# Kernel tuning notes

Measured on AMD Instinct MI355X. Metric: run time of the kernel, lower is better.

## Reference

```python
import jax, jax.numpy as jnp
import numpy as np

N_NODES = 50000
N_EDGES = 600000
IN_CH = 300
HID = 128
N_CLASSES = 2
N_GRAPHS = 128
BN_EPS = 1e-5


def setup_inputs() -> dict:
    key = jax.random.key(0)
    ks = jax.random.split(key, 24)
    x = jax.random.normal(ks[0], (N_NODES, IN_CH), dtype=jnp.float32)
    edge_index = jax.random.randint(ks[1], (2, N_EDGES), 0, N_NODES, dtype=jnp.int64)
    batch = jnp.sort(jax.random.randint(ks[2], (N_NODES,), 0, N_GRAPHS, dtype=jnp.int64))

    def glorot(k, shape):
        fan_in, fan_out = shape
        s = jnp.sqrt(2.0 / (fan_in + fan_out)).astype(jnp.float32)
        return jax.random.normal(k, shape, dtype=jnp.float32) * s

    inp = {"x": x, "edge_index": edge_index, "batch": batch}
    # SAGEConv params: W_l (neighbor branch), W_r (root branch), bias
    dims = [(IN_CH, HID), (HID, HID), (HID, HID)]
    for i, (din, dout) in enumerate(dims, start=1):
        inp[f"W{i}l"] = glorot(ks[3 * i], (din, dout))
        inp[f"W{i}r"] = glorot(ks[3 * i + 1], (din, dout))
        inp[f"b{i}"] = jnp.zeros((dout,), dtype=jnp.float32)
        inp[f"g{i}"] = jnp.ones((dout,), dtype=jnp.float32)   # BN gamma
        inp[f"be{i}"] = jnp.zeros((dout,), dtype=jnp.float32)  # BN beta
    inp["Wc"] = glorot(ks[20], (HID, N_CLASSES))
    inp["bc"] = jnp.zeros((N_CLASSES,), dtype=jnp.float32)
    return inp


def _sage_conv(x, src, dst, Wl, Wr, b):
    # mean-aggregate neighbor features (messages flow src -> dst)
    msg_sum = jax.ops.segment_sum(x[src], dst, num_segments=N_NODES)
    deg = jax.ops.segment_sum(jnp.ones((src.shape[0],), dtype=x.dtype), dst,
                              num_segments=N_NODES)
    mean = msg_sum / jnp.maximum(deg, 1.0)[:, None]
    return mean @ Wl + x @ Wr + b


def _bn_relu(h, gamma, beta):
    mu = jnp.mean(h, axis=0)
    var = jnp.var(h, axis=0)
    h = (h - mu) * jax.lax.rsqrt(var + BN_EPS) * gamma + beta
    return jax.nn.relu(h)


def reference(x, edge_index, batch,
              W1l, W1r, b1, g1, be1,
              W2l, W2r, b2, g2, be2,
              W3l, W3r, b3, g3, be3,
              Wc, bc):
    src, dst = edge_index[0], edge_index[1]
    h = _bn_relu(_sage_conv(x, src, dst, W1l, W1r, b1), g1, be1)
    h = _bn_relu(_sage_conv(h, src, dst, W2l, W2r, b2), g2, be2)
    h = _bn_relu(_sage_conv(h, src, dst, W3l, W3r, b3), g3, be3)
    # global mean pool per graph
    pooled = jax.ops.segment_sum(h, batch, num_segments=N_GRAPHS)
    cnt = jax.ops.segment_sum(jnp.ones((h.shape[0],), dtype=h.dtype), batch,
                              num_segments=N_GRAPHS)
    hg = pooled / jnp.maximum(cnt, 1.0)[:, None]
    out = hg @ Wc + bc
    return out, hg
```

## Files before the change

kernel.cpp:

```cpp
#include <hip/hip_runtime.h>

#define N_NODES   50000
#define N_EDGES   600000
#define IN_CH     300
#define HID       128
#define N_CLASSES 2
#define N_GRAPHS  128
#define BN_EPS    1e-5f

#define NB ((N_NODES + 511) / 512)
#define KP1 320
#define NREP 32
#define DEGB ((N_EDGES + 255) / 256)

typedef __attribute__((ext_vector_type(8))) short bf8_t;
typedef __attribute__((ext_vector_type(4))) float f4_t;

__device__ __forceinline__ unsigned short f2bf(float x) {
    union { float f; unsigned u; } q; q.f = x;
    unsigned r = q.u + 0x7fffu + ((q.u >> 16) & 1u);
    return (unsigned short)(r >> 16);
}
__device__ __forceinline__ float bf2f(unsigned short h) {
    union { float f; unsigned u; } q; q.u = ((unsigned)h) << 16; return q.f;
}

__device__ __forceinline__ void async_cp16(const void* g, void* l) {
    __builtin_amdgcn_global_load_lds(
        (const __attribute__((address_space(1))) unsigned int*)g,
        (__attribute__((address_space(3))) unsigned int*)l, 16, 0, 0);
}

__global__ __launch_bounds__(256) void deg_prepw(const int* __restrict__ dst,
                                                 int* __restrict__ ideg,
                                                 const float* __restrict__ W1l,
                                                 const float* __restrict__ W1r,
                                                 const float* __restrict__ W2l,
                                                 const float* __restrict__ W2r,
                                                 const float* __restrict__ W3l,
                                                 const float* __restrict__ W3r,
                                                 unsigned short* __restrict__ B1h,
                                                 unsigned short* __restrict__ B1l,
                                                 unsigned short* __restrict__ B2h,
                                                 unsigned short* __restrict__ B2l,
                                                 unsigned short* __restrict__ B3h,
                                                 unsigned short* __restrict__ B3l) {
    int b = blockIdx.x;
    if (b < DEGB) {
        int e = b * 256 + threadIdx.x;
        if (e < N_EDGES) atomicAdd(&ideg[dst[e]], 1);
        return;
    }
    int pb = b - DEGB;
    int layer, base;
    if (pb < 320)      { layer = 0; base = pb; }
    else if (pb < 448) { layer = 1; base = pb - 320; }
    else               { layer = 2; base = pb - 448; }
    int Kp = (layer == 0) ? KP1 : HID;
    int K  = (layer == 0) ? IN_CH : HID;
    const float* Wl = (layer == 0) ? W1l : ((layer == 1) ? W2l : W3l);
    const float* Wr = (layer == 0) ? W1r : ((layer == 1) ? W2r : W3r);
    unsigned short* Bh = (layer == 0) ? B1h : ((layer == 1) ? B2h : B3h);
    unsigned short* Bl = (layer == 0) ? B1l : ((layer == 1) ? B2l : B3l);
    int idx = base * 256 + threadIdx.x;
    int n = idx / Kp;
    int k = idx - n * Kp;
    float v = 0.f;
    if (k < K) v = (n < 128) ? Wl[k * 128 + n] : Wr[k * 128 + (n - 128)];
    unsigned short h = f2bf(v);
    unsigned short l = f2bf(v - bf2f(h));
    Bh[idx] = h;
    Bl[idx] = l;
}

__global__ __launch_bounds__(256) void scan_fused(const int* __restrict__ ideg,
                                                  int* __restrict__ row_start,
                                                  float* __restrict__ invdeg,
                                                  int* __restrict__ bsum,
                                                  int* __restrict__ bflag) {
    int b = blockIdx.x, t = threadIdx.x;
    int lane = t & 63, wv = t >> 6;
    int i0 = b * 512 + t * 2;
    int v0 = 0, v1 = 0;
    if (i0 < N_NODES) {
        int2 v = *(const int2*)&ideg[i0];
        v0 = v.x; v1 = v.y;
    }
    int tot = v0 + v1;
    int s = tot;
#pragma unroll
    for (int d = 1; d < 64; d <<= 1) {
        int u = __shfl_up(s, d);
        if (lane >= d) s += u;
    }
    __shared__ int ws[4];
    if (lane == 63) ws[wv] = s;
    __syncthreads();
    int btot = ws[0] + ws[1] + ws[2] + ws[3];
    if (t == 0) {
        atomicExch(&bsum[b], btot);
        __threadfence();
        atomicExch(&bflag[b], 1);
    }
    int part = 0;
    if (t < b) {
        while (atomicAdd(&bflag[t], 0) == 0) {}
        part = atomicAdd(&bsum[t], 0);
    }
#pragma unroll
    for (int d = 1; d < 64; d <<= 1) part += __shfl_down(part, d);
    __shared__ int ps[4];
    if (lane == 0) ps[wv] = part;
    __syncthreads();
    int boff = ps[0] + ps[1] + ps[2] + ps[3];
    int woff = 0;
    for (int w = 0; w < wv; ++w) woff += ws[w];
    int base = boff + woff + (s - tot);
    if (i0 < N_NODES) {
        row_start[i0]     = base;
        row_start[i0 + 1] = base + v0;
        invdeg[i0]     = 1.0f / fmaxf((float)v0, 1.0f);
        invdeg[i0 + 1] = 1.0f / fmaxf((float)v1, 1.0f);
    }
    if (t == 0 && b == NB - 1) row_start[N_NODES] = boff + btot;
}

__global__ __launch_bounds__(256) void fill_kernel(const int* __restrict__ src,
                                                   const int* __restrict__ dst,
                                                   const int* __restrict__ row_start,
                                                   int* __restrict__ cursor,
                                                   int* __restrict__ csr_src) {
    int e = blockIdx.x * 256 + threadIdx.x;
    if (e >= N_EDGES) return;
    int d = dst[e];
    int pos = row_start[d] + atomicAdd(&cursor[d], 1);
    csr_src[pos] = src[e];
}

__global__ __launch_bounds__(256) void gemm_mfma_x(const float* __restrict__ X,
                                                   int M,
                                                   const unsigned short* __restrict__ Bhi,
                                                   const unsigned short* __restrict__ Blo,
                                                   const float* __restrict__ bias,
                                                   unsigned short* __restrict__ C0,
                                                   float* __restrict__ C1) {
    __shared__ __align__(16) unsigned short sAh[2][64 * 32];
    __shared__ __align__(16) unsigned short sAl[2][64 * 32];
    __shared__ __align__(16) unsigned short sBh[2][256 * 32];
    __shared__ __align__(16) unsigned short sBl[2][256 * 32];

    const int tid  = threadIdx.x;
    const int lane = tid & 63;
    const int wave = tid >> 6;
    const int l16  = lane & 15;
    const int quad = lane >> 4;
    const long m0  = (long)blockIdx.x * 64;
    const int  n0  = wave * 64;

    f4_t acc[4][4];
#pragma unroll
    for (int mt = 0; mt < 4; ++mt)
#pragma unroll
        for (int nt = 0; nt < 4; ++nt) acc[mt][nt] = (f4_t){0.f, 0.f, 0.f, 0.f};

    const int ar  = tid >> 2;
    const int cl  = tid & 3;
    const int cpa = cl ^ ((ar >> 1) & 3);
    long agr = m0 + ar;
    if (agr >= M) agr = M - 1;
    const float* gX = X + agr * IN_CH;

    const int cg = ((lane & 3) ^ ((lane >> 3) & 3)) * 8;
    const unsigned short* gBh[4];
    const unsigned short* gBl[4];
    int lBo[4];
#pragma unroll
    for (int j = 0; j < 4; ++j) {
        long br = wave * 64 + j * 16 + (lane >> 2);
        gBh[j] = Bhi + br * KP1 + cg;
        gBl[j] = Blo + br * KP1 + cg;
        lBo[j] = wave * 2048 + j * 512;
    }
    const int rsw = (quad ^ ((l16 >> 1) & 3)) * 8;

    auto copyB = [&](int k0, int buf) {
#pragma unroll
        for (int j = 0; j < 4; ++j) {
            async_cp16(gBh[j] + k0, &sBh[buf][lBo[j]]);
            async_cp16(gBl[j] + k0, &sBl[buf][lBo[j]]);
        }
    };
    auto loadA = [&](int k0, float4& a0, float4& a1) {
        int gk = k0 + cl * 8;
        a0 = (gk + 4 <= IN_CH) ? *(const float4*)(gX + gk)
                               : make_float4(0.f, 0.f, 0.f, 0.f);
        a1 = (gk + 8 <= IN_CH) ? *(const float4*)(gX + gk + 4)
                               : make_float4(0.f, 0.f, 0.f, 0.f);
    };
    auto storeA = [&](int buf, float4 a0, float4 a1) {
        float f[8];
        f[0] = a0.x; f[1] = a0.y; f[2] = a0.z; f[3] = a0.w;
        f[4] = a1.x; f[5] = a1.y; f[6] = a1.z; f[7] = a1.w;
        bf8_t h8, l8;
#pragma unroll
        for (int j = 0; j < 8; ++j) {
            unsigned short h = f2bf(f[j]);
            h8[j] = (short)h;
            l8[j] = (short)f2bf(f[j] - bf2f(h));
        }
        *(bf8_t*)&sAh[buf][ar * 32 + cpa * 8] = h8;
        *(bf8_t*)&sAl[buf][ar * 32 + cpa * 8] = l8;
    };

    {
        float4 a0, a1;
        loadA(0, a0, a1);
        copyB(0, 0);
        storeA(0, a0, a1);
    }
    __syncthreads();

    const int NT = KP1 / 32;
    int cur = 0;
    for (int t = 0; t < NT; ++t) {
        float4 na0 = make_float4(0.f, 0.f, 0.f, 0.f);
        float4 na1 = make_float4(0.f, 0.f, 0.f, 0.f);
        const bool more = (t + 1 < NT);
        if (more) {
            loadA((t + 1) * 32, na0, na1);
            copyB((t + 1) * 32, cur ^ 1);
        }

        bf8_t ah[4], al[4];
#pragma unroll
        for (int mt = 0; mt < 4; ++mt) {
            ah[mt] = *(const bf8_t*)&sAh[cur][(mt * 16 + l16) * 32 + rsw];
            al[mt] = *(const bf8_t*)&sAl[cur][(mt * 16 + l16) * 32 + rsw];
        }
#pragma unroll
        for (int nt = 0; nt < 4; ++nt) {
            bf8_t bh = *(const bf8_t*)&sBh[cur][(n0 + nt * 16 + l16) * 32 + rsw];
            bf8_t bl = *(const bf8_t*)&sBl[cur][(n0 + nt * 16 + l16) * 32 + rsw];
#pragma unroll
            for (int mt = 0; mt < 4; ++mt) {
                acc[mt][nt] = __builtin_amdgcn_mfma_f32_16x16x32_bf16(ah[mt], bh, acc[mt][nt], 0, 0, 0);
                acc[mt][nt] = __builtin_amdgcn_mfma_f32_16x16x32_bf16(al[mt], bh, acc[mt][nt], 0, 0, 0);
                acc[mt][nt] = __builtin_amdgcn_mfma_f32_16x16x32_bf16(ah[mt], bl, acc[mt][nt], 0, 0, 0);
            }
        }

        if (more) storeA(cur ^ 1, na0, na1);
        __syncthreads();
        cur ^= 1;
    }

    const bool left = (n0 < 128);
    if (left) {
        int ncol[4];
#pragma unroll
        for (int nt = 0; nt < 4; ++nt) ncol[nt] = n0 + nt * 16 + l16;
#pragma unroll
        for (int mt = 0; mt < 4; ++mt)
#pragma unroll
            for (int r = 0; r < 4; ++r) {
                long row = m0 + mt * 16 + quad * 4 + r;
                if (row < M) {
#pragma unroll
                    for (int nt = 0; nt < 4; ++nt)
                        C0[row * 128 + ncol[nt]] = f2bf(acc[mt][nt][r]);
                }
            }
    } else {
        float badd[4];
        int   ncol[4];
#pragma unroll
        for (int nt = 0; nt < 4; ++nt) {
            int ng = n0 + nt * 16 + l16 - 128;
            ncol[nt] = ng;
            badd[nt] = bias[ng];
        }
#pragma unroll
        for (int mt = 0; mt < 4; ++mt)
#pragma unroll
            for (int r = 0; r < 4; ++r) {
                long row = m0 + mt * 16 + quad * 4 + r;
                if (row < M) {
#pragma unroll
                    for (int nt = 0; nt < 4; ++nt)
                        C1[row * 128 + ncol[nt]] = acc[mt][nt][r] + badd[nt];
                }
            }
    }
}

__global__ __launch_bounds__(256) void gemm_mfma_h(const float* __restrict__ Hpre,
                                                   int M,
                                                   const float* __restrict__ rep,
                                                   const float* __restrict__ gamma,
                                                   const float* __restrict__ beta,
                                                   const unsigned short* __restrict__ Bhi,
                                                   const unsigned short* __restrict__ Blo,
                                                   const float* __restrict__ bias,
                                                   unsigned short* __restrict__ C0,
                                                   float* __restrict__ C1) {
    __shared__ __align__(16) unsigned short sAh[64 * 32];
    __shared__ __align__(16) unsigned short sAl[64 * 32];
    __shared__ __align__(16) unsigned short sBh[2][256 * 32];
    __shared__ __align__(16) unsigned short sBl[2][256 * 32];
    __shared__ float sSC[256];

    const int tid  = threadIdx.x;
    const int lane = tid & 63;
    const int wave = tid >> 6;
    const int l16  = lane & 15;
    const int quad = lane >> 4;
    const long m0  = (long)blockIdx.x * 64;
    const int  n0  = wave * 64;

    {
        float* S = (float*)sAh;
        float a = 0.f;
#pragma unroll
        for (int r = 0; r < NREP; ++r) a += rep[r * 256 + tid];
        S[tid] = a;
        __syncthreads();
        if (tid < HID) {
            const float invn = 1.0f / (float)N_NODES;
            float mu  = S[tid] * invn;
            float var = S[HID + tid] * invn - mu * mu;
            float sc  = gamma[tid] * rsqrtf(var + BN_EPS);
            sSC[tid]       = sc;
            sSC[HID + tid] = beta[tid] - mu * sc;
        }
        __syncthreads();
    }

    f4_t acc[4][4];
#pragma unroll
    for (int mt = 0; mt < 4; ++mt)
#pragma unroll
        for (int nt = 0; nt < 4; ++nt) acc[mt][nt] = (f4_t){0.f, 0.f, 0.f, 0.f};

    const int ar  = tid >> 2;
    const int cl  = tid & 3;
    const int cpa = cl ^ ((ar >> 1) & 3);
    long agr = m0 + ar;
    if (agr >= M) agr = M - 1;
    const float* gH = Hpre + agr * HID;

    const int cg = ((lane & 3) ^ ((lane >> 3) & 3)) * 8;
    const unsigned short* gBh[4];
    const unsigned short* gBl[4];
    int lBo[4];
#pragma unroll
    for (int j = 0; j < 4; ++j) {
        long br = wave * 64 + j * 16 + (lane >> 2);
        gBh[j] = Bhi + br * HID + cg;
        gBl[j] = Blo + br * HID + cg;
        lBo[j] = wave * 2048 + j * 512;
    }
    const int rsw = (quad ^ ((l16 >> 1) & 3)) * 8;

    auto copyB = [&](int k0, int buf) {
#pragma unroll
        for (int j = 0; j < 4; ++j) {
            async_cp16(gBh[j] + k0, &sBh[buf][lBo[j]]);
            async_cp16(gBl[j] + k0, &sBl[buf][lBo[j]]);
        }
    };
    auto loadA = [&](int k0, float4& a0, float4& a1) {
        int gk = k0 + cl * 8;
        a0 = *(const float4*)(gH + gk);
        a1 = *(const float4*)(gH + gk + 4);
    };
    auto storeA = [&](int k0, float4 v0, float4 v1) {
        const int gk = k0 + cl * 8;
        float4 s0 = *(const float4*)&sSC[gk];
        float4 s1 = *(const float4*)&sSC[gk + 4];
        float4 t0 = *(const float4*)&sSC[HID + gk];
        float4 t1 = *(const float4*)&sSC[HID + gk + 4];
        float f[8];
        f[0] = fmaxf(v0.x * s0.x + t0.x, 0.f);
        f[1] = fmaxf(v0.y * s0.y + t0.y, 0.f);
        f[2] = fmaxf(v0.z * s0.z + t0.z, 0.f);
        f[3] = fmaxf(v0.w * s0.w + t0.w, 0.f);
        f[4] = fmaxf(v1.x * s1.x + t1.x, 0.f);
        f[5] = fmaxf(v1.y * s1.y + t1.y, 0.f);
        f[6] = fmaxf(v1.z * s1.z + t1.z, 0.f);
        f[7] = fmaxf(v1.w * s1.w + t1.w, 0.f);
        bf8_t h8, l8;
#pragma unroll
        for (int j = 0; j < 8; ++j) {
            unsigned short h = f2bf(f[j]);
            h8[j] = (short)h;
            l8[j] = (short)f2bf(f[j] - bf2f(h));
        }
        *(bf8_t*)&sAh[ar * 32 + cpa * 8] = h8;
        *(bf8_t*)&sAl[ar * 32 + cpa * 8] = l8;
    };

    {
        float4 a0, a1;
        loadA(0, a0, a1);
        copyB(0, 0);
        storeA(0, a0, a1);
    }
    __syncthreads();

    int cur = 0;
#pragma unroll
    for (int t = 0; t < 4; ++t) {
        float4 na0 = make_float4(0.f, 0.f, 0.f, 0.f);
        float4 na1 = make_float4(0.f, 0.f, 0.f, 0.f);
        const bool more = (t < 3);
        if (more) {
            loadA((t + 1) * 32, na0, na1);
            copyB((t + 1) * 32, cur ^ 1);
        }

        bf8_t ah[4], al[4];
#pragma unroll
        for (int mt = 0; mt < 4; ++mt) {
            ah[mt] = *(const bf8_t*)&sAh[(mt * 16 + l16) * 32 + rsw];
            al[mt] = *(const bf8_t*)&sAl[(mt * 16 + l16) * 32 + rsw];
        }
#pragma unroll
        for (int nt = 0; nt < 4; ++nt) {
            bf8_t bh = *(const bf8_t*)&sBh[cur][(n0 + nt * 16 + l16) * 32 + rsw];
            bf8_t bl = *(const bf8_t*)&sBl[cur][(n0 + nt * 16 + l16) * 32 + rsw];
#pragma unroll
            for (int mt = 0; mt < 4; ++mt) {
                acc[mt][nt] = __builtin_amdgcn_mfma_f32_16x16x32_bf16(ah[mt], bh, acc[mt][nt], 0, 0, 0);
                acc[mt][nt] = __builtin_amdgcn_mfma_f32_16x16x32_bf16(al[mt], bh, acc[mt][nt], 0, 0, 0);
                acc[mt][nt] = __builtin_amdgcn_mfma_f32_16x16x32_bf16(ah[mt], bl, acc[mt][nt], 0, 0, 0);
            }
        }

        __syncthreads();
        if (more) storeA((t + 1) * 32, na0, na1);
        __syncthreads();
        cur ^= 1;
    }

    const bool left = (n0 < 128);
    if (left) {
        int ncol[4];
#pragma unroll
        for (int nt = 0; nt < 4; ++nt) ncol[nt] = n0 + nt * 16 + l16;
#pragma unroll
        for (int mt = 0; mt < 4; ++mt)
#pragma unroll
            for (int r = 0; r < 4; ++r) {
                long row = m0 + mt * 16 + quad * 4 + r;
                if (row < M) {
#pragma unroll
                    for (int nt = 0; nt < 4; ++nt)
                        C0[row * 128 + ncol[nt]] = f2bf(acc[mt][nt][r]);
                }
            }
    } else {
        float badd[4];
        int   ncol[4];
#pragma unroll
        for (int nt = 0; nt < 4; ++nt) {
            int ng = n0 + nt * 16 + l16 - 128;
            ncol[nt] = ng;
            badd[nt] = bias[ng];
        }
#pragma unroll
        for (int mt = 0; mt < 4; ++mt)
#pragma unroll
            for (int r = 0; r < 4; ++r) {
                long row = m0 + mt * 16 + quad * 4 + r;
                if (row < M) {
#pragma unroll
                    for (int nt = 0; nt < 4; ++nt)
                        C1[row * 128 + ncol[nt]] = acc[mt][nt][r] + badd[nt];
                }
            }
    }
}

__global__ __launch_bounds__(256) void gather_agg(const unsigned short* __restrict__ Pl,
                                                  const int* __restrict__ row_start,
                                                  const int* __restrict__ csr_src,
                                                  const float* __restrict__ invdeg,
                                                  float* __restrict__ out,
                                                  float* __restrict__ rep) {
    int slot = threadIdx.x >> 5;
    int lane = threadIdx.x & 31;
    int node = blockIdx.x * 8 + slot;
    int beg = row_start[node];
    int end = row_start[node + 1];
    const unsigned short* base = Pl + lane * 4;
    float sx = 0.f, sy = 0.f, sz = 0.f, sw = 0.f;
    int j = beg;
    for (; j + 8 <= end; j += 8) {
        int idx[8];
#pragma unroll
        for (int u = 0; u < 8; ++u) idx[u] = csr_src[j + u];
        ushort4 v[8];
#pragma unroll
        for (int u = 0; u < 8; ++u) v[u] = *(const ushort4*)(base + (long)idx[u] * HID);
#pragma unroll
        for (int u = 0; u < 8; ++u) {
            sx += bf2f(v[u].x); sy += bf2f(v[u].y);
            sz += bf2f(v[u].z); sw += bf2f(v[u].w);
        }
    }
    if (j + 4 <= end) {
        int idx[4];
#pragma unroll
        for (int u = 0; u < 4; ++u) idx[u] = csr_src[j + u];
        ushort4 v[4];
#pragma unroll
        for (int u = 0; u < 4; ++u) v[u] = *(const ushort4*)(base + (long)idx[u] * HID);
#pragma unroll
        for (int u = 0; u < 4; ++u) {
            sx += bf2f(v[u].x); sy += bf2f(v[u].y);
            sz += bf2f(v[u].z); sw += bf2f(v[u].w);
        }
        j += 4;
    }
    for (; j < end; ++j) {
        int i0 = csr_src[j];
        ushort4 v0 = *(const ushort4*)(base + (long)i0 * HID);
        sx += bf2f(v0.x); sy += bf2f(v0.y); sz += bf2f(v0.z); sw += bf2f(v0.w);
    }
    float w = invdeg[node];
    float* o = out + (long)node * HID + lane * 4;
    float4 cur = *(float4*)o;
    cur.x += sx * w;
    cur.y += sy * w;
    cur.z += sz * w;
    cur.w += sw * w;
    *(float4*)o = cur;

    __shared__ float red[8][HID];
    float* repb = rep + (blockIdx.x & (NREP - 1)) * 256;
    *(float4*)&red[slot][lane * 4] = make_float4(cur.x, cur.y, cur.z, cur.w);
    __syncthreads();
    if (threadIdx.x < HID) {
        float tsum = 0.f;
#pragma unroll
        for (int s = 0; s < 8; ++s) tsum += red[s][threadIdx.x];
        atomicAdd(&repb[threadIdx.x], tsum);
    }
    __syncthreads();
    *(float4*)&red[slot][lane * 4] = make_float4(cur.x * cur.x, cur.y * cur.y,
                                                 cur.z * cur.z, cur.w * cur.w);
    __syncthreads();
    if (threadIdx.x < HID) {
        float tsum = 0.f;
#pragma unroll
        for (int s = 0; s < 8; ++s) tsum += red[s][threadIdx.x];
        atomicAdd(&repb[HID + threadIdx.x], tsum);
    }
}

__global__ __launch_bounds__(1024) void poolhead_bn(const float* __restrict__ h,
                                                    const int* __restrict__ batch,
                                                    const float* __restrict__ rep,
                                                    const float* __restrict__ gamma,
                                                    const float* __restrict__ beta,
                                                    const float* __restrict__ Wc,
                                                    const float* __restrict__ bc,
                                                    float* __restrict__ out) {
    __shared__ float S[256];
    __shared__ float SC[256];
    int g = blockIdx.x;
    int t = threadIdx.x;
    int c = t & 127;
    int half = t >> 7;
    if (t < 256) {
        float a = 0.f;
#pragma unroll
        for (int r = 0; r < NREP; ++r) a += rep[r * 256 + t];
        S[t] = a;
    }
    __shared__ int lo_sh, hi_sh;
    if (t == 0) {
        int lo = 0, hi = N_NODES;
        while (lo < hi) { int m = (lo + hi) >> 1; if (batch[m] < g) lo = m + 1; else hi = m; }
        lo_sh = lo;
        int lo2 = lo, hi2 = N_NODES;
        while (lo2 < hi2) { int m = (lo2 + hi2) >> 1; if (batch[m] < g + 1) lo2 = m + 1; else hi2 = m; }
        hi_sh = lo2;
    }
    __syncthreads();
    if (t < HID) {
        const float invn = 1.0f / (float)N_NODES;
        float mu  = S[t] * invn;
        float var = S[HID + t] * invn - mu * mu;
        float sc  = gamma[t] * rsqrtf(var + BN_EPS);
        SC[t]       = sc;
        SC[HID + t] = beta[t] - mu * sc;
    }
    __syncthreads();
    float bsc = SC[c], bsh = SC[HID + c];
    int lo = lo_sh, hi = hi_sh;
    float a0 = 0.f, a1 = 0.f, a2 = 0.f, a3 = 0.f;
    int r = lo + half;
    for (; r + 24 < hi; r += 32) {
        a0 += fmaxf(h[(long)(r +  0) * HID + c] * bsc + bsh, 0.f);
        a1 += fmaxf(h[(long)(r +  8) * HID + c] * bsc + bsh, 0.f);
        a2 += fmaxf(h[(long)(r + 16) * HID + c] * bsc + bsh, 0.f);
        a3 += fmaxf(h[(long)(r + 24) * HID + c] * bsc + bsh, 0.f);
    }
    for (; r < hi; r += 8) a0 += fmaxf(h[(long)r * HID + c] * bsc + bsh, 0.f);
    __shared__ float red[8][HID];
    red[half][c] = (a0 + a1) + (a2 + a3);
    __syncthreads();
    __shared__ float r0[HID], r1[HID];
    if (t < HID) {
        float inv = 1.0f / fmaxf((float)(hi - lo), 1.0f);
        float v = 0.f;
#pragma unroll
        for (int s = 0; s < 8; ++s) v += red[s][t];
        v *= inv;
        out[N_GRAPHS * N_CLASSES + g * HID + t] = v;
        r0[t] = v * Wc[t * 2 + 0];
        r1[t] = v * Wc[t * 2 + 1];
    }
    __syncthreads();
    if (t < 2) {
        const float* rr = t ? r1 : r0;
        float sum = bc[t];
        for (int i = 0; i < HID; ++i) sum += rr[i];
        out[g * 2 + t] = sum;
    }
}

extern "C" void kernel_launch(void* const* d_in, const int* in_sizes, int n_in,
                              void* d_out, int out_size, void* d_ws, size_t ws_size,
                              hipStream_t stream) {
    const float* x     = (const float*)d_in[0];
    const int*   ei    = (const int*)d_in[1];
    const int*   batch = (const int*)d_in[2];
    const float* W1l = (const float*)d_in[3];
    const float* W1r = (const float*)d_in[4];
    const float* b1  = (const float*)d_in[5];
    const float* g1  = (const float*)d_in[6];
    const float* be1 = (const float*)d_in[7];
    const float* W2l = (const float*)d_in[8];
    const float* W2r = (const float*)d_in[9];
    const float* b2  = (const float*)d_in[10];
    const float* g2  = (const float*)d_in[11];
    const float* be2 = (const float*)d_in[12];
    const float* W3l = (const float*)d_in[13];
    const float* W3r = (const float*)d_in[14];
    const float* b3  = (const float*)d_in[15];
    const float* g3  = (const float*)d_in[16];
    const float* be3 = (const float*)d_in[17];
    const float* Wc  = (const float*)d_in[18];
    const float* bc  = (const float*)d_in[19];

    const int* src = ei;
    const int* dst = ei + N_EDGES;

    float* ws = (float*)d_ws;
    const long FEAT = (long)N_NODES * HID;
    unsigned short* Pl16 = (unsigned short*)ws;
    float* buf1 = ws + FEAT;
    float* buf2 = ws + 2 * FEAT;
    int*   ideg      = (int*)(ws + 3 * FEAT);
    int*   cursor    = ideg + N_NODES;
    int*   bsum      = cursor + N_NODES;
    int*   bflag     = bsum + 128;
    int*   row_start = bflag + 128;
    int*   csr_src   = row_start + N_NODES + 4;
    float* invdeg    = (float*)(csr_src + N_EDGES);
    float* reps      = invdeg + N_NODES;
    unsigned short* B1h = (unsigned short*)(reps + 3 * NREP * 256);
    unsigned short* B1l = B1h + 256 * KP1;
    unsigned short* B2h = B1l + 256 * KP1;
    unsigned short* B2l = B2h + 256 * HID;
    unsigned short* B3h = B2l + 256 * HID;
    unsigned short* B3l = B3h + 256 * HID;

    float* outp = (float*)d_out;

    const int gemm_grid   = (N_NODES + 63) / 64;
    const int gather_grid = N_NODES / 8;
    const int dp_grid     = DEGB + 320 + 128 + 128;

    hipMemsetAsync(ideg, 0, (2 * N_NODES + 256) * sizeof(int), stream);
    hipMemsetAsync(reps, 0, 3 * NREP * 256 * sizeof(float), stream);

    deg_prepw<<<dp_grid, 256, 0, stream>>>(dst, ideg, W1l, W1r, W2l, W2r, W3l, W3r,
                                           B1h, B1l, B2h, B2l, B3h, B3l);
    scan_fused<<<NB, 256, 0, stream>>>(ideg, row_start, invdeg, bsum, bflag);
    fill_kernel<<<(N_EDGES + 255) / 256, 256, 0, stream>>>(src, dst, row_start, cursor, csr_src);

    gemm_mfma_x<<<gemm_grid, 256, 0, stream>>>(x, N_NODES, B1h, B1l, b1, Pl16, buf1);
    gather_agg<<<gather_grid, 256, 0, stream>>>(Pl16, row_start, csr_src, invdeg, buf1, reps);

    gemm_mfma_h<<<gemm_grid, 256, 0, stream>>>(buf1, N_NODES, reps, g1, be1,
                                               B2h, B2l, b2, Pl16, buf2);
    gather_agg<<<gather_grid, 256, 0, stream>>>(Pl16, row_start, csr_src, invdeg, buf2, reps + NREP * 256);

    gemm_mfma_h<<<gemm_grid, 256, 0, stream>>>(buf2, N_NODES, reps + NREP * 256, g2, be2,
                                               B3h, B3l, b3, Pl16, buf1);
    gather_agg<<<gather_grid, 256, 0, stream>>>(Pl16, row_start, csr_src, invdeg, buf1, reps + 2 * NREP * 256);

    poolhead_bn<<<N_GRAPHS, 1024, 0, stream>>>(buf1, batch, reps + 2 * NREP * 256,
                                               g3, be3, Wc, bc, outp);
}
```

Baseline: 404.1 us.

## Pre-swizzle weights into MFMA fragment layout and load B directly from global

```diff
diff --git a/kernel.cpp b/kernel.cpp
--- a/kernel.cpp
+++ b/kernel.cpp
@@ -23,12 +23,6 @@
 }
 __device__ __forceinline__ float bf2f(unsigned short h) {
     union { float f; unsigned u; } q; q.u = ((unsigned)h) << 16; return q.f;
-}
-
-__device__ __forceinline__ void async_cp16(const void* g, void* l) {
-    __builtin_amdgcn_global_load_lds(
-        (const __attribute__((address_space(1))) unsigned int*)g,
-        (__attribute__((address_space(3))) unsigned int*)l, 16, 0, 0);
 }
 
 __global__ __launch_bounds__(256) void deg_prepw(const int* __restrict__ dst,
@@ -69,8 +63,15 @@
     if (k < K) v = (n < 128) ? Wl[k * 128 + n] : Wr[k * 128 + (n - 128)];
     unsigned short h = f2bf(v);
     unsigned short l = f2bf(v - bf2f(h));
-    Bh[idx] = h;
-    Bl[idx] = l;
+    int NST   = Kp >> 5;
+    int ntile = n >> 4;
+    int l16n  = n & 15;
+    int kstep = k >> 5;
+    int kk    = k & 31;
+    int lane2 = (kk >> 3) * 16 + l16n;
+    int addr  = ((ntile * NST + kstep) * 64 + lane2) * 8 + (kk & 7);
+    Bh[addr] = h;
+    Bl[addr] = l;
 }
 
 __global__ __launch_bounds__(256) void scan_fused(const int* __restrict__ ideg,
@@ -146,8 +147,6 @@
                                                    float* __restrict__ C1) {
     __shared__ __align__(16) unsigned short sAh[2][64 * 32];
     __shared__ __align__(16) unsigned short sAl[2][64 * 32];
-    __shared__ __align__(16) unsigned short sBh[2][256 * 32];
-    __shared__ __align__(16) unsigned short sBl[2][256 * 32];
 
     const int tid  = threadIdx.x;
     const int lane = tid & 63;
@@ -170,26 +169,12 @@
     if (agr >= M) agr = M - 1;
     const float* gX = X + agr * IN_CH;
 
-    const int cg = ((lane & 3) ^ ((lane >> 3) & 3)) * 8;
-    const unsigned short* gBh[4];
-    const unsigned short* gBl[4];
-    int lBo[4];
-#pragma unroll
-    for (int j = 0; j < 4; ++j) {
-        long br = wave * 64 + j * 16 + (lane >> 2);
-        gBh[j] = Bhi + br * KP1 + cg;
-        gBl[j] = Blo + br * KP1 + cg;
-        lBo[j] = wave * 2048 + j * 512;
-    }
     const int rsw = (quad ^ ((l16 >> 1) & 3)) * 8;
-
-    auto copyB = [&](int k0, int buf) {
-#pragma unroll
-        for (int j = 0; j < 4; ++j) {
-            async_cp16(gBh[j] + k0, &sBh[buf][lBo[j]]);
-            async_cp16(gBl[j] + k0, &sBl[buf][lBo[j]]);
-        }
-    };
+    const int NT  = KP1 / 32;
+
+    const bf8_t* Bh0 = (const bf8_t*)Bhi;
+    const bf8_t* Bl0 = (const bf8_t*)Blo;
+
     auto loadA = [&](int k0, float4& a0, float4& a1) {
         int gk = k0 + cl * 8;
         a0 = (gk + 4 <= IN_CH) ? *(const float4*)(gX + gk)
@@ -215,20 +200,23 @@
     {
         float4 a0, a1;
         loadA(0, a0, a1);
-        copyB(0, 0);
         storeA(0, a0, a1);
     }
     __syncthreads();
 
-    const int NT = KP1 / 32;
     int cur = 0;
     for (int t = 0; t < NT; ++t) {
         float4 na0 = make_float4(0.f, 0.f, 0.f, 0.f);
         float4 na1 = make_float4(0.f, 0.f, 0.f, 0.f);
         const bool more = (t + 1 < NT);
-        if (more) {
-            loadA((t + 1) * 32, na0, na1);
-            copyB((t + 1) * 32, cur ^ 1);
+        if (more) loadA((t + 1) * 32, na0, na1);
+
+        bf8_t bhv[4], blv[4];
+#pragma unroll
+        for (int nt = 0; nt < 4; ++nt) {
+            long bi = ((long)(wave * 4 + nt) * NT + t) * 64 + lane;
+            bhv[nt] = Bh0[bi];
+            blv[nt] = Bl0[bi];
         }
 
         bf8_t ah[4], al[4];
@@ -239,13 +227,11 @@
         }
 #pragma unroll
         for (int nt = 0; nt < 4; ++nt) {
-            bf8_t bh = *(const bf8_t*)&sBh[cur][(n0 + nt * 16 + l16) * 32 + rsw];
-            bf8_t bl = *(const bf8_t*)&sBl[cur][(n0 + nt * 16 + l16) * 32 + rsw];
 #pragma unroll
             for (int mt = 0; mt < 4; ++mt) {
-                acc[mt][nt] = __builtin_amdgcn_mfma_f32_16x16x32_bf16(ah[mt], bh, acc[mt][nt], 0, 0, 0);
-                acc[mt][nt] = __builtin_amdgcn_mfma_f32_16x16x32_bf16(al[mt], bh, acc[mt][nt], 0, 0, 0);
-                acc[mt][nt] = __builtin_amdgcn_mfma_f32_16x16x32_bf16(ah[mt], bl, acc[mt][nt], 0, 0, 0);
+                acc[mt][nt] = __builtin_amdgcn_mfma_f32_16x16x32_bf16(ah[mt], bhv[nt], acc[mt][nt], 0, 0, 0);
+                acc[mt][nt] = __builtin_amdgcn_mfma_f32_16x16x32_bf16(al[mt], bhv[nt], acc[mt][nt], 0, 0, 0);
+                acc[mt][nt] = __builtin_amdgcn_mfma_f32_16x16x32_bf16(ah[mt], blv[nt], acc[mt][nt], 0, 0, 0);
             }
         }
 
@@ -303,10 +289,8 @@
                                                    const float* __restrict__ bias,
                                                    unsigned short* __restrict__ C0,
                                                    float* __restrict__ C1) {
-    __shared__ __align__(16) unsigned short sAh[64 * 32];
-    __shared__ __align__(16) unsigned short sAl[64 * 32];
-    __shared__ __align__(16) unsigned short sBh[2][256 * 32];
-    __shared__ __align__(16) unsigned short sBl[2][256 * 32];
+    __shared__ __align__(16) unsigned short sAh[2][64 * 32];
+    __shared__ __align__(16) unsigned short sAl[2][64 * 32];
     __shared__ float sSC[256];
 
     const int tid  = threadIdx.x;
@@ -348,32 +332,18 @@
     if (agr >= M) agr = M - 1;
     const float* gH = Hpre + agr * HID;
 
-    const int cg = ((lane & 3) ^ ((lane >> 3) & 3)) * 8;
-    const unsigned short* gBh[4];
-    const unsigned short* gBl[4];
-    int lBo[4];
-#pragma unroll
-    for (int j = 0; j < 4; ++j) {
-        long br = wave * 64 + j * 16 + (lane >> 2);
-        gBh[j] = Bhi + br * HID + cg;
-        gBl[j] = Blo + br * HID + cg;
-        lBo[j] = wave * 2048 + j * 512;
-    }
     const int rsw = (quad ^ ((l16 >> 1) & 3)) * 8;
-
-    auto copyB = [&](int k0, int buf) {
-#pragma unroll
-        for (int j = 0; j < 4; ++j) {
-            async_cp16(gBh[j] + k0, &sBh[buf][lBo[j]]);
-            async_cp16(gBl[j] + k0, &sBl[buf][lBo[j]]);
-        }
-    };
+    const int NT  = HID / 32;
+
+    const bf8_t* Bh0 = (const bf8_t*)Bhi;
+    const bf8_t* Bl0 = (const bf8_t*)Blo;
+
     auto loadA = [&](int k0, float4& a0, float4& a1) {
         int gk = k0 + cl * 8;
         a0 = *(const float4*)(gH + gk);
         a1 = *(const float4*)(gH + gk + 4);
     };
-    auto storeA = [&](int k0, float4 v0, float4 v1) {
+    auto storeA = [&](int buf, int k0, float4 v0, float4 v1) {
         const int gk = k0 + cl * 8;
         float4 s0 = *(const float4*)&sSC[gk];
         float4 s1 = *(const float4*)&sSC[gk + 4];
@@ -395,15 +365,14 @@
             h8[j] = (short)h;
             l8[j] = (short)f2bf(f[j] - bf2f(h));
         }
-        *(bf8_t*)&sAh[ar * 32 + cpa * 8] = h8;
-        *(bf8_t*)&sAl[ar * 32 + cpa * 8] = l8;
+        *(bf8_t*)&sAh[buf][ar * 32 + cpa * 8] = h8;
+        *(bf8_t*)&sAl[buf][ar * 32 + cpa * 8] = l8;
     };
 
     {
         float4 a0, a1;
         loadA(0, a0, a1);
-        copyB(0, 0);
-        storeA(0, a0, a1);
+        storeA(0, 0, a0, a1);
     }
     __syncthreads();
 
@@ -413,31 +382,33 @@
         float4 na0 = make_float4(0.f, 0.f, 0.f, 0.f);
         float4 na1 = make_float4(0.f, 0.f, 0.f, 0.f);
         const bool more = (t < 3);
-        if (more) {
-            loadA((t + 1) * 32, na0, na1);
-            copyB((t + 1) * 32, cur ^ 1);
+        if (more) loadA((t + 1) * 32, na0, na1);
+
+        bf8_t bhv[4], blv[4];
+#pragma unroll
+        for (int nt = 0; nt < 4; ++nt) {
+            long bi = ((long)(wave * 4 + nt) * NT + t) * 64 + lane;
+            bhv[nt] = Bh0[bi];
+            blv[nt] = Bl0[bi];
         }
 
         bf8_t ah[4], al[4];
 #pragma unroll
         for (int mt = 0; mt < 4; ++mt) {
-            ah[mt] = *(const bf8_t*)&sAh[(mt * 16 + l16) * 32 + rsw];
-            al[mt] = *(const bf8_t*)&sAl[(mt * 16 + l16) * 32 + rsw];
+            ah[mt] = *(const bf8_t*)&sAh[cur][(mt * 16 + l16) * 32 + rsw];
+            al[mt] = *(const bf8_t*)&sAl[cur][(mt * 16 + l16) * 32 + rsw];
         }
 #pragma unroll
         for (int nt = 0; nt < 4; ++nt) {
-            bf8_t bh = *(const bf8_t*)&sBh[cur][(n0 + nt * 16 + l16) * 32 + rsw];
-            bf8_t bl = *(const bf8_t*)&sBl[cur][(n0 + nt * 16 + l16) * 32 + rsw];
 #pragma unroll
             for (int mt = 0; mt < 4; ++mt) {
-                acc[mt][nt] = __builtin_amdgcn_mfma_f32_16x16x32_bf16(ah[mt], bh, acc[mt][nt], 0, 0, 0);
-                acc[mt][nt] = __builtin_amdgcn_mfma_f32_16x16x32_bf16(al[mt], bh, acc[mt][nt], 0, 0, 0);
-                acc[mt][nt] = __builtin_amdgcn_mfma_f32_16x16x32_bf16(ah[mt], bl, acc[mt][nt], 0, 0, 0);
+                acc[mt][nt] = __builtin_amdgcn_mfma_f32_16x16x32_bf16(ah[mt], bhv[nt], acc[mt][nt], 0, 0, 0);
+                acc[mt][nt] = __builtin_amdgcn_mfma_f32_16x16x32_bf16(al[mt], bhv[nt], acc[mt][nt], 0, 0, 0);
+                acc[mt][nt] = __builtin_amdgcn_mfma_f32_16x16x32_bf16(ah[mt], blv[nt], acc[mt][nt], 0, 0, 0);
             }
         }
 
-        __syncthreads();
-        if (more) storeA((t + 1) * 32, na0, na1);
+        if (more) storeA(cur ^ 1, (t + 1) * 32, na0, na1);
         __syncthreads();
         cur ^= 1;
     }
```

Measured after the change: 386.6 us. 1.05x faster.
